# Kernel optimization log

Hardware: AMD Instinct MI355X
Metric: run time of the kernel (lower is better)

Reference implementation:

```python
import jax, jax.numpy as jnp
import numpy as np

N_NODES = 100000
N_EDGES = 1600000
FEATURE = 32
HIDDEN = 64
CLASSES = 10
K = 3  # TAGConv default number of hops


def setup_inputs() -> dict:
    key = jax.random.key(0)
    k1, k2, k3, k4, k5, k6, k7 = jax.random.split(key, 7)
    x = jax.random.normal(k1, (N_NODES, FEATURE), dtype=jnp.float32)
    edge_index = jax.random.randint(k2, (2, N_EDGES), 0, N_NODES, dtype=jnp.int32)
    # TAGConv holds K+1 linear maps (one per hop power) plus a bias.
    s1 = 1.0 / np.sqrt(FEATURE)
    s2 = 1.0 / np.sqrt(HIDDEN)
    W1 = jax.random.uniform(k3, (K + 1, FEATURE, HIDDEN), jnp.float32, -s1, s1)
    b1 = jax.random.uniform(k4, (HIDDEN,), jnp.float32, -s1, s1)
    W2 = jax.random.uniform(k5, (K + 1, HIDDEN, CLASSES), jnp.float32, -s2, s2)
    b2 = jax.random.uniform(k6, (CLASSES,), jnp.float32, -s2, s2)
    return {"x": x, "edge_index": edge_index, "W1": W1, "b1": b1, "W2": W2, "b2": b2}


def _tagconv(x, row, col, norm, W, b):
    # out = sum_k (A_hat^k x) W_k + b, A_hat = D^-1/2 A D^-1/2 (no self loops)
    out = x @ W[0]
    h = x
    for k in range(1, W.shape[0]):
        h = jnp.zeros_like(h).at[col].add(norm[:, None] * h[row])
        out = out + h @ W[k]
    return out + b


def reference(x, edge_index, W1, b1, W2, b2):
    row, col = edge_index[0], edge_index[1]
    n = x.shape[0]
    # gcn_norm with unit edge weights, add_self_loops=False
    deg = jnp.zeros((n,), x.dtype).at[col].add(1.0)
    dinv = jnp.where(deg > 0, jax.lax.rsqrt(jnp.maximum(deg, 1.0)), 0.0)
    norm = dinv[row] * dinv[col]

    h = _tagconv(x, row, col, norm, W1, b1)
    h = jax.nn.relu(h)
    # dropout is identity in eval mode
    h = _tagconv(h, row, col, norm, W2, b2)
    return jax.nn.log_softmax(h, axis=1)
```

## Files before the change

### kernel.cpp

```cpp
#include <hip/hip_runtime.h>

typedef unsigned int uint;
typedef short s8v __attribute__((ext_vector_type(8)));
typedef float f4v __attribute__((ext_vector_type(4)));

#define N_NODES 100000
#define N_EDGES 1600000
#define FEAT 32
#define HID 64
#define NCLS 10

#define BUCKET_SHIFT 8
#define NBUCKET 391
#define NCB 256
#define CHUNK ((N_EDGES + NCB - 1) / NCB)
#define BH_N (NBUCKET * NCB)
#define NB_BH ((BH_N + 255) / 256)
#define CAP 6144
#define LROW 65


__device__ __forceinline__ uint pack_bf16(float lo, float hi) {
    uint a = __float_as_uint(lo);
    uint b = __float_as_uint(hi);
    a = a + 0x7fffu + ((a >> 16) & 1u);
    b = b + 0x7fffu + ((b >> 16) & 1u);
    return (a >> 16) | (b & 0xffff0000u);
}
__device__ __forceinline__ float unp_lo(uint v) { return __uint_as_float(v << 16); }
__device__ __forceinline__ float unp_hi(uint v) { return __uint_as_float(v & 0xffff0000u); }

__device__ __forceinline__ s8v to_s8(uint4 u) {
    union { uint4 u; s8v s; } x;
    x.u = u;
    return x.s;
}


__global__ void bucket_hist(const int* __restrict__ col, int* __restrict__ blockhist) {
    __shared__ int lh[NBUCKET];
    int blk = blockIdx.x;
    for (int i = threadIdx.x; i < NBUCKET; i += 256) lh[i] = 0;
    __syncthreads();
    int e0 = blk * CHUNK;
    int e1 = min(e0 + CHUNK, N_EDGES);
    for (int e = e0 + threadIdx.x; e < e1; e += 256)
        atomicAdd(&lh[col[e] >> BUCKET_SHIFT], 1);
    __syncthreads();
    for (int i = threadIdx.x; i < NBUCKET; i += 256)
        blockhist[i * NCB + blk] = lh[i];
}

__global__ void scanA_kernel(const int* __restrict__ src, int* __restrict__ dst,
                             int* __restrict__ bsum, int n) {
    __shared__ int s[256];
    int gid = blockIdx.x * 256 + threadIdx.x;
    int v = (gid < n) ? src[gid] : 0;
    s[threadIdx.x] = v;
    __syncthreads();
    for (int off = 1; off < 256; off <<= 1) {
        int t = (threadIdx.x >= off) ? s[threadIdx.x - off] : 0;
        __syncthreads();
        s[threadIdx.x] += t;
        __syncthreads();
    }
    if (gid < n) dst[gid] = s[threadIdx.x] - v;
    if (threadIdx.x == 255) bsum[blockIdx.x] = s[255];
}

__global__ void scanB_kernel(int* __restrict__ bsum, int nb) {
    __shared__ int s[512];
    int v = (threadIdx.x < nb) ? bsum[threadIdx.x] : 0;
    s[threadIdx.x] = v;
    __syncthreads();
    for (int off = 1; off < 512; off <<= 1) {
        int t = (threadIdx.x >= off) ? s[threadIdx.x - off] : 0;
        __syncthreads();
        s[threadIdx.x] += t;
        __syncthreads();
    }
    if (threadIdx.x < nb) bsum[threadIdx.x] = s[threadIdx.x] - v;
}

__global__ void scanC_add(int* __restrict__ dst, const int* __restrict__ bsum, int n) {
    int gid = blockIdx.x * 256 + threadIdx.x;
    if (gid < n) dst[gid] += bsum[blockIdx.x];
}

__global__ void bucket_scatter(const int* __restrict__ row, const int* __restrict__ col,
                               const int* __restrict__ base, int* __restrict__ packed) {
    __shared__ int lcnt[NBUCKET];
    __shared__ int lbase[NBUCKET];
    int blk = blockIdx.x;
    for (int i = threadIdx.x; i < NBUCKET; i += 256) {
        lcnt[i] = 0;
        lbase[i] = base[i * NCB + blk];
    }
    __syncthreads();
    int e0 = blk * CHUNK;
    int e1 = min(e0 + CHUNK, N_EDGES);
    for (int e = e0 + threadIdx.x; e < e1; e += 256) {
        int c = col[e];
        int r = row[e];
        int b = c >> BUCKET_SHIFT;
        int pos = lbase[b] + atomicAdd(&lcnt[b], 1);
        packed[pos] = (r << BUCKET_SHIFT) | (c & 255);
    }
}

__global__ void bucket_sort(const int* __restrict__ base, const int* __restrict__ packed,
                            int* __restrict__ rowptr, int* __restrict__ eidx,
                            float* __restrict__ dinv) {
    __shared__ int stage[CAP];
    __shared__ int cnt[256];
    __shared__ int lscan[256];
    int b = blockIdx.x;
    int tid = threadIdx.x;
    int s = base[b * NCB];
    int e = (b == NBUCKET - 1) ? N_EDGES : base[(b + 1) * NCB];
    int m = e - s;
    bool fits = (m <= CAP);
    cnt[tid] = 0;
    __syncthreads();
    for (int i = tid; i < m; i += 256) {
        int p = packed[s + i];
        if (fits) stage[i] = p;
        atomicAdd(&cnt[p & 255], 1);
    }
    __syncthreads();
    int node = (b << BUCKET_SHIFT) + tid;
    int c = cnt[tid];
    if (node < N_NODES) dinv[node] = (c > 0) ? rsqrtf((float)c) : 0.0f;
    lscan[tid] = c;
    __syncthreads();
    for (int off = 1; off < 256; off <<= 1) {
        int t = (tid >= off) ? lscan[tid - off] : 0;
        __syncthreads();
        lscan[tid] += t;
        __syncthreads();
    }
    int excl = lscan[tid] - c;
    if (node < N_NODES) rowptr[node] = s + excl;
    if (b == NBUCKET - 1 && tid == 0) rowptr[N_NODES] = N_EDGES;
    __syncthreads();
    lscan[tid] = excl;
    cnt[tid] = 0;
    __syncthreads();
    for (int i = tid; i < m; i += 256) {
        int p = fits ? stage[i] : packed[s + i];
        int cl = p & 255;
        int pos = lscan[cl] + atomicAdd(&cnt[cl], 1);
        eidx[s + pos] = p >> BUCKET_SHIFT;
    }
}


__global__ void prescale_kernel(const float* __restrict__ x, const float* __restrict__ dinv,
                                uint* __restrict__ t0) {
    int i = blockIdx.x * 256 + threadIdx.x;
    if (i < N_NODES * 16) {
        int node = i >> 4, fp = i & 15;
        float dv = dinv[node];
        t0[i] = pack_bf16(x[node * 32 + 2 * fp] * dv, x[node * 32 + 2 * fp + 1] * dv);
    }
}


template <int WP>
__global__ void gather32_kernel(const int* __restrict__ rowptr, const int* __restrict__ eidx,
                                const float* __restrict__ dinv, const uint* __restrict__ src,
                                uint* __restrict__ pout, uint* __restrict__ preout) {
    int node = (blockIdx.x * blockDim.x + threadIdx.x) >> 6;
    if (node >= N_NODES) return;
    int lane = threadIdx.x & 63;
    int fp = lane & 15;
    int g = lane >> 4;
    int s = rowptr[node], e = rowptr[node + 1];
    float acc0 = 0.0f, acc1 = 0.0f;
    int base = (s & ~3) + g * 4;
    for (int b = base; b < e; b += 16) {
        int4 q = *(const int4*)(eidx + b);
        uint v0 = (b     >= s && b     < e) ? src[q.x * 16 + fp] : 0u;
        uint v1 = (b + 1 >= s && b + 1 < e) ? src[q.y * 16 + fp] : 0u;
        uint v2 = (b + 2 >= s && b + 2 < e) ? src[q.z * 16 + fp] : 0u;
        uint v3 = (b + 3 >= s && b + 3 < e) ? src[q.w * 16 + fp] : 0u;
        acc0 += unp_lo(v0) + unp_lo(v1) + unp_lo(v2) + unp_lo(v3);
        acc1 += unp_hi(v0) + unp_hi(v1) + unp_hi(v2) + unp_hi(v3);
    }
    acc0 += __shfl_xor(acc0, 16);
    acc0 += __shfl_xor(acc0, 32);
    acc1 += __shfl_xor(acc1, 16);
    acc1 += __shfl_xor(acc1, 32);
    if (lane < 16) {
        float dv = dinv[node];
        pout[node * 16 + fp] = pack_bf16(dv * acc0, dv * acc1);
        if (WP) {
            float d2 = dv * dv;
            preout[node * 16 + fp] = pack_bf16(d2 * acc0, d2 * acc1);
        }
    }
}

template <int FINAL>
__global__ void gather16_kernel(const int* __restrict__ rowptr, const int* __restrict__ eidx,
                                const float* __restrict__ dinv, const float* __restrict__ src,
                                const float* __restrict__ add, float* __restrict__ outv) {
    int node = (blockIdx.x * blockDim.x + threadIdx.x) >> 6;
    if (node >= N_NODES) return;
    int lane = threadIdx.x & 63;
    int f = lane & 15;
    int g = lane >> 4;
    int s = rowptr[node], e = rowptr[node + 1];
    float acc = 0.0f;
    int base = (s & ~3) + g * 4;
    for (int b = base; b < e; b += 16) {
        int4 q = *(const int4*)(eidx + b);
        float v0 = (b     >= s && b     < e) ? src[q.x * 16 + f] : 0.0f;
        float v1 = (b + 1 >= s && b + 1 < e) ? src[q.y * 16 + f] : 0.0f;
        float v2 = (b + 2 >= s && b + 2 < e) ? src[q.z * 16 + f] : 0.0f;
        float v3 = (b + 3 >= s && b + 3 < e) ? src[q.w * 16 + f] : 0.0f;
        acc += v0 + v1 + v2 + v3;
    }
    acc += __shfl_xor(acc, 16);
    acc += __shfl_xor(acc, 32);
    float dv = dinv[node];
    float v = add[node * 16 + f] + dv * acc;
    if (!FINAL) {
        if (lane < 16) outv[node * 16 + f] = dv * v;
    } else {
        float l = (f < NCLS) ? v : -1e30f;
        float m = l;
        m = fmaxf(m, __shfl_xor(m, 1));
        m = fmaxf(m, __shfl_xor(m, 2));
        m = fmaxf(m, __shfl_xor(m, 4));
        m = fmaxf(m, __shfl_xor(m, 8));
        float ex = (f < NCLS) ? __expf(l - m) : 0.0f;
        ex += __shfl_xor(ex, 1);
        ex += __shfl_xor(ex, 2);
        ex += __shfl_xor(ex, 4);
        ex += __shfl_xor(ex, 8);
        float ls = logf(ex) + m;
        if (lane < 16 && f < NCLS) outv[node * NCLS + f] = l - ls;
    }
}


__global__ void wfprep_kernel(const float* __restrict__ W1, const float* __restrict__ W2,
                              uint* __restrict__ wf1, uint* __restrict__ wf2) {
    int idx = blockIdx.x * 256 + threadIdx.x;
    if (idx < 4096) {
        int vj = idx & 3, frag = idx >> 2;
        int lane = frag & 63, ks = (frag >> 6) & 3, nt = frag >> 8;
        int g = lane >> 4, c = lane & 15;
        int k0 = ks * 32 + g * 8 + 2 * vj;
        int n = nt * 16 + c;
        wf1[idx] = pack_bf16(W1[k0 * 64 + n], W1[(k0 + 1) * 64 + n]);
    } else if (idx < 6144) {
        int i2 = idx - 4096;
        int vj = i2 & 3, frag = i2 >> 2;
        int lane = frag & 63, ks = (frag >> 6) & 1, nt = frag >> 7;
        int g = lane >> 4, c = lane & 15;
        int k0 = ks * 32 + g * 8 + 2 * vj;
        float v0 = (c < NCLS) ? W2[(nt * HID + k0) * NCLS + c] : 0.0f;
        float v1 = (c < NCLS) ? W2[(nt * HID + k0 + 1) * NCLS + c] : 0.0f;
        wf2[i2] = pack_bf16(v0, v1);
    }
}


__global__ __launch_bounds__(256) void dense_fused(
        const float* __restrict__ x, const uint* __restrict__ p1,
        const uint* __restrict__ p2, const uint* __restrict__ p3,
        const uint* __restrict__ wf1, const uint* __restrict__ wf2,
        const float* __restrict__ b1, const float* __restrict__ b2,
        const float* __restrict__ dinv, float* __restrict__ z, int zstride) {
    __shared__ float hls[4 * 16 * LROW];
    int tid = threadIdx.x;
    int wv = tid >> 6, l = tid & 63, g = l >> 4, c = l & 15;
    float* my = hls + wv * 16 * LROW;
    int row0 = blockIdx.x * 64 + wv * 16;
    int ra = row0 + c;
    int rc = min(ra, N_NODES - 1);

    uint4 au0;
    {
        float4 xa = *(const float4*)(x + rc * 32 + g * 8);
        float4 xb = *(const float4*)(x + rc * 32 + g * 8 + 4);
        au0.x = pack_bf16(xa.x, xa.y);
        au0.y = pack_bf16(xa.z, xa.w);
        au0.z = pack_bf16(xb.x, xb.y);
        au0.w = pack_bf16(xb.z, xb.w);
    }
    uint4 au1 = *(const uint4*)(p1 + rc * 16 + g * 4);
    uint4 au2 = *(const uint4*)(p2 + rc * 16 + g * 4);
    uint4 au3 = *(const uint4*)(p3 + rc * 16 + g * 4);
    s8v a0 = to_s8(au0), a1 = to_s8(au1), a2 = to_s8(au2), a3 = to_s8(au3);

    f4v acc[4];
#pragma unroll
    for (int nt = 0; nt < 4; nt++) {
        f4v ac = {0.f, 0.f, 0.f, 0.f};
        const s8v* wp = (const s8v*)(wf1 + (nt * 4) * 64 * 4 + l * 4);
        ac = __builtin_amdgcn_mfma_f32_16x16x32_bf16(a0, wp[0 * 64], ac, 0, 0, 0);
        ac = __builtin_amdgcn_mfma_f32_16x16x32_bf16(a1, wp[1 * 64], ac, 0, 0, 0);
        ac = __builtin_amdgcn_mfma_f32_16x16x32_bf16(a2, wp[2 * 64], ac, 0, 0, 0);
        ac = __builtin_amdgcn_mfma_f32_16x16x32_bf16(a3, wp[3 * 64], ac, 0, 0, 0);
        acc[nt] = ac;
    }

#pragma unroll
    for (int nt = 0; nt < 4; nt++) {
        float bb = b1[nt * 16 + c];
#pragma unroll
        for (int reg = 0; reg < 4; reg++) {
            my[(4 * g + reg) * LROW + nt * 16 + c] = fmaxf(acc[nt][reg] + bb, 0.0f);
        }
    }
    __syncthreads();

    uint4 b2u[2];
#pragma unroll
    for (int ks = 0; ks < 2; ks++) {
        float4 h0 = *(const float4*)&my[c * LROW + ks * 32 + g * 8];
        float4 h1 = *(const float4*)&my[c * LROW + ks * 32 + g * 8 + 4];
        b2u[ks].x = pack_bf16(h0.x, h0.y);
        b2u[ks].y = pack_bf16(h0.z, h0.w);
        b2u[ks].z = pack_bf16(h1.x, h1.y);
        b2u[ks].w = pack_bf16(h1.z, h1.w);
    }
    s8v h0f = to_s8(b2u[0]), h1f = to_s8(b2u[1]);

    f4v acc2[4];
#pragma unroll
    for (int nt = 0; nt < 4; nt++) {
        f4v ac = {0.f, 0.f, 0.f, 0.f};
        const s8v* wp = (const s8v*)(wf2 + (nt * 2) * 64 * 4 + l * 4);
        ac = __builtin_amdgcn_mfma_f32_16x16x32_bf16(h0f, wp[0 * 64], ac, 0, 0, 0);
        ac = __builtin_amdgcn_mfma_f32_16x16x32_bf16(h1f, wp[1 * 64], ac, 0, 0, 0);
        acc2[nt] = ac;
    }

#pragma unroll
    for (int nt = 0; nt < 4; nt++) {
        float bb = (nt == 0 && c < NCLS) ? b2[c] : 0.0f;
        float* zk = z + (size_t)nt * zstride;
#pragma unroll
        for (int reg = 0; reg < 4; reg++) {
            int rr = row0 + 4 * g + reg;
            if (rr < N_NODES) {
                float v = acc2[nt][reg] + bb;
                if (nt == 3) v *= dinv[rr];
                zk[rr * 16 + c] = v;
            }
        }
    }
}


extern "C" void kernel_launch(void* const* d_in, const int* in_sizes, int n_in,
                              void* d_out, int out_size, void* d_ws, size_t ws_size,
                              hipStream_t stream) {
    const float* x  = (const float*)d_in[0];
    const int*   ei = (const int*)d_in[1];
    const float* W1 = (const float*)d_in[2];
    const float* b1 = (const float*)d_in[3];
    const float* W2 = (const float*)d_in[4];
    const float* b2 = (const float*)d_in[5];
    float* out = (float*)d_out;

    const int* row = ei;
    const int* col = ei + N_EDGES;

    float* w = (float*)d_ws;
    size_t o = 0;
    auto alloc = [&](size_t nel) { float* p = w + o; o += (nel + 63) & ~(size_t)63; return p; };

    int*   rowptr = (int*)alloc(N_NODES + 1);
    int*   bsum   = (int*)alloc(512);
    float* dinv   = alloc(N_NODES);
    uint*  wf1    = (uint*)alloc(4096);
    uint*  wf2    = (uint*)alloc(2048);
    int*   eidx   = (int*)alloc(N_EDGES + 16);
    float* bufA   = alloc((size_t)N_NODES * 32);
    float* bufB   = alloc((size_t)N_NODES * 32);
    float* bufC   = alloc((size_t)N_NODES * 32);
    float* bufD   = alloc((size_t)N_NODES * 32);
    float* h      = alloc((size_t)N_NODES * HID);

    int* blockhist = (int*)bufB;
    int* bhbase    = (int*)bufC;
    int* packed    = (int*)h;

    uint* t0  = (uint*)bufA;
    uint* p1  = (uint*)bufB;
    uint* p1p = (uint*)bufC;
    uint* p2  = (uint*)bufD;
    uint* p2p = (uint*)bufA;
    uint* p3  = (uint*)bufC;
    const int ZS = N_NODES * 16;
    float* z0  = h;
    float* z1  = h + ZS;
    float* z2  = h + 2 * (size_t)ZS;
    float* z3p = h + 3 * (size_t)ZS;
    float* tAp = bufC;
    float* tBp = bufC + ZS;

    const int TB = 256;
    const int gW = (N_NODES * 64) / TB;

    bucket_hist<<<NCB, TB, 0, stream>>>(col, blockhist);
    scanA_kernel<<<NB_BH, TB, 0, stream>>>(blockhist, bhbase, bsum, BH_N);
    scanB_kernel<<<1, 512, 0, stream>>>(bsum, NB_BH);
    scanC_add<<<NB_BH, TB, 0, stream>>>(bhbase, bsum, BH_N);
    bucket_scatter<<<NCB, TB, 0, stream>>>(row, col, bhbase, packed);
    bucket_sort<<<NBUCKET, TB, 0, stream>>>(bhbase, packed, rowptr, eidx, dinv);

    wfprep_kernel<<<24, TB, 0, stream>>>(W1, W2, wf1, wf2);

    prescale_kernel<<<(N_NODES * 16 + TB - 1) / TB, TB, 0, stream>>>(x, dinv, t0);
    gather32_kernel<1><<<gW, TB, 0, stream>>>(rowptr, eidx, dinv, t0,  p1, p1p);
    gather32_kernel<1><<<gW, TB, 0, stream>>>(rowptr, eidx, dinv, p1p, p2, p2p);
    gather32_kernel<0><<<gW, TB, 0, stream>>>(rowptr, eidx, dinv, p2p, p3, nullptr);

    int gF = (N_NODES + 63) / 64;
    dense_fused<<<gF, TB, 0, stream>>>(x, p1, p2, p3, wf1, wf2, b1, b2, dinv, z0, ZS);

    gather16_kernel<0><<<gW, TB, 0, stream>>>(rowptr, eidx, dinv, z3p, z2, tAp);
    gather16_kernel<0><<<gW, TB, 0, stream>>>(rowptr, eidx, dinv, tAp, z1, tBp);
    gather16_kernel<1><<<gW, TB, 0, stream>>>(rowptr, eidx, dinv, tBp, z0, out);
}
```

Before: 346.4 us.

## Store layer-2 propagation buffers in bf16 and pack two nodes per wave

The 16-wide layer-2 intermediates (z0..z3 and the gather ping-pong buffers) are now stored as packed bf16 pairs instead of fp32, halving the bytes moved by the three 16-channel gathers. Each gather wave now processes two nodes with 8 lanes per node, each lane handling two channels, so half as many waves are launched. The dense kernel packs neighbouring-lane outputs with a shuffle before storing. This trades some precision in the output logits for less memory traffic in the random-access gathers.

```diff
diff --git a/kernel.cpp b/kernel.cpp
--- a/kernel.cpp
+++ b/kernel.cpp
@@ -203,44 +203,53 @@
 
 template <int FINAL>
 __global__ void gather16_kernel(const int* __restrict__ rowptr, const int* __restrict__ eidx,
-                                const float* __restrict__ dinv, const float* __restrict__ src,
-                                const float* __restrict__ add, float* __restrict__ outv) {
-    int node = (blockIdx.x * blockDim.x + threadIdx.x) >> 6;
+                                const float* __restrict__ dinv, const uint* __restrict__ src,
+                                const uint* __restrict__ add, void* __restrict__ outv) {
+    int wid = (blockIdx.x * blockDim.x + threadIdx.x) >> 6;
+    int lane = threadIdx.x & 63;
+    int node = wid * 2 + (lane >> 5);
     if (node >= N_NODES) return;
-    int lane = threadIdx.x & 63;
-    int f = lane & 15;
-    int g = lane >> 4;
+    int fp = lane & 7;
+    int g = (lane >> 3) & 3;
     int s = rowptr[node], e = rowptr[node + 1];
-    float acc = 0.0f;
+    float acc0 = 0.0f, acc1 = 0.0f;
     int base = (s & ~3) + g * 4;
     for (int b = base; b < e; b += 16) {
         int4 q = *(const int4*)(eidx + b);
-        float v0 = (b     >= s && b     < e) ? src[q.x * 16 + f] : 0.0f;
-        float v1 = (b + 1 >= s && b + 1 < e) ? src[q.y * 16 + f] : 0.0f;
-        float v2 = (b + 2 >= s && b + 2 < e) ? src[q.z * 16 + f] : 0.0f;
-        float v3 = (b + 3 >= s && b + 3 < e) ? src[q.w * 16 + f] : 0.0f;
-        acc += v0 + v1 + v2 + v3;
-    }
-    acc += __shfl_xor(acc, 16);
-    acc += __shfl_xor(acc, 32);
+        uint v0 = (b     >= s && b     < e) ? src[q.x * 8 + fp] : 0u;
+        uint v1 = (b + 1 >= s && b + 1 < e) ? src[q.y * 8 + fp] : 0u;
+        uint v2 = (b + 2 >= s && b + 2 < e) ? src[q.z * 8 + fp] : 0u;
+        uint v3 = (b + 3 >= s && b + 3 < e) ? src[q.w * 8 + fp] : 0u;
+        acc0 += unp_lo(v0) + unp_lo(v1) + unp_lo(v2) + unp_lo(v3);
+        acc1 += unp_hi(v0) + unp_hi(v1) + unp_hi(v2) + unp_hi(v3);
+    }
+    acc0 += __shfl_xor(acc0, 8);
+    acc0 += __shfl_xor(acc0, 16);
+    acc1 += __shfl_xor(acc1, 8);
+    acc1 += __shfl_xor(acc1, 16);
     float dv = dinv[node];
-    float v = add[node * 16 + f] + dv * acc;
+    uint av = add[node * 8 + fp];
+    float v0 = unp_lo(av) + dv * acc0;
+    float v1 = unp_hi(av) + dv * acc1;
     if (!FINAL) {
-        if (lane < 16) outv[node * 16 + f] = dv * v;
+        if (g == 0) ((uint*)outv)[node * 8 + fp] = pack_bf16(dv * v0, dv * v1);
     } else {
-        float l = (f < NCLS) ? v : -1e30f;
-        float m = l;
+        float l0 = (2 * fp     < NCLS) ? v0 : -1e30f;
+        float l1 = (2 * fp + 1 < NCLS) ? v1 : -1e30f;
+        float m = fmaxf(l0, l1);
         m = fmaxf(m, __shfl_xor(m, 1));
         m = fmaxf(m, __shfl_xor(m, 2));
         m = fmaxf(m, __shfl_xor(m, 4));
-        m = fmaxf(m, __shfl_xor(m, 8));
-        float ex = (f < NCLS) ? __expf(l - m) : 0.0f;
+        float ex = ((2 * fp     < NCLS) ? __expf(l0 - m) : 0.0f)
+                 + ((2 * fp + 1 < NCLS) ? __expf(l1 - m) : 0.0f);
         ex += __shfl_xor(ex, 1);
         ex += __shfl_xor(ex, 2);
         ex += __shfl_xor(ex, 4);
-        ex += __shfl_xor(ex, 8);
         float ls = logf(ex) + m;
-        if (lane < 16 && f < NCLS) outv[node * NCLS + f] = l - ls;
+        if (g == 0 && fp < 5) {
+            float2 o = {l0 - ls, l1 - ls};
+            *(float2*)((float*)outv + (size_t)node * 10 + 2 * fp) = o;
+        }
     }
 }
 
@@ -273,7 +282,7 @@
         const uint* __restrict__ p2, const uint* __restrict__ p3,
         const uint* __restrict__ wf1, const uint* __restrict__ wf2,
         const float* __restrict__ b1, const float* __restrict__ b2,
-        const float* __restrict__ dinv, float* __restrict__ z, int zstride) {
+        const float* __restrict__ dinv, uint* __restrict__ z, int zstride) {
     __shared__ float hls[4 * 16 * LROW];
     int tid = threadIdx.x;
     int wv = tid >> 6, l = tid & 63, g = l >> 4, c = l & 15;
@@ -343,14 +352,15 @@
 #pragma unroll
     for (int nt = 0; nt < 4; nt++) {
         float bb = (nt == 0 && c < NCLS) ? b2[c] : 0.0f;
-        float* zk = z + (size_t)nt * zstride;
+        uint* zk = z + (size_t)nt * zstride;
 #pragma unroll
         for (int reg = 0; reg < 4; reg++) {
             int rr = row0 + 4 * g + reg;
-            if (rr < N_NODES) {
-                float v = acc2[nt][reg] + bb;
-                if (nt == 3) v *= dinv[rr];
-                zk[rr * 16 + c] = v;
+            float v = acc2[nt][reg] + bb;
+            if (nt == 3) v *= dinv[min(rr, N_NODES - 1)];
+            float vn = __shfl_xor(v, 1);
+            if (rr < N_NODES && (c & 1) == 0) {
+                zk[rr * 8 + (c >> 1)] = pack_bf16(v, vn);
             }
         }
     }
@@ -397,16 +407,17 @@
     uint* p2  = (uint*)bufD;
     uint* p2p = (uint*)bufA;
     uint* p3  = (uint*)bufC;
-    const int ZS = N_NODES * 16;
-    float* z0  = h;
-    float* z1  = h + ZS;
-    float* z2  = h + 2 * (size_t)ZS;
-    float* z3p = h + 3 * (size_t)ZS;
-    float* tAp = bufC;
-    float* tBp = bufC + ZS;
+    const int ZS = N_NODES * 8;
+    uint* z0  = (uint*)h;
+    uint* z1  = (uint*)h + ZS;
+    uint* z2  = (uint*)h + 2 * (size_t)ZS;
+    uint* z3p = (uint*)h + 3 * (size_t)ZS;
+    uint* tAp = (uint*)bufC;
+    uint* tBp = (uint*)bufC + ZS;
 
     const int TB = 256;
     const int gW = (N_NODES * 64) / TB;
+    const int gW2 = ((N_NODES + 1) / 2 * 64 + TB - 1) / TB;
 
     bucket_hist<<<NCB, TB, 0, stream>>>(col, blockhist);
     scanA_kernel<<<NB_BH, TB, 0, stream>>>(blockhist, bhbase, bsum, BH_N);
@@ -425,7 +436,7 @@
     int gF = (N_NODES + 63) / 64;
     dense_fused<<<gF, TB, 0, stream>>>(x, p1, p2, p3, wf1, wf2, b1, b2, dinv, z0, ZS);
 
-    gather16_kernel<0><<<gW, TB, 0, stream>>>(rowptr, eidx, dinv, z3p, z2, tAp);
-    gather16_kernel<0><<<gW, TB, 0, stream>>>(rowptr, eidx, dinv, tAp, z1, tBp);
-    gather16_kernel<1><<<gW, TB, 0, stream>>>(rowptr, eidx, dinv, tBp, z0, out);
-}
+    gather16_kernel<0><<<gW2, TB, 0, stream>>>(rowptr, eidx, dinv, z3p, z2, tAp);
+    gather16_kernel<0><<<gW2, TB, 0, stream>>>(rowptr, eidx, dinv, tAp, z1, tBp);
+    gather16_kernel<1><<<gW2, TB, 0, stream>>>(rowptr, eidx, dinv, tBp, z0, out);
+}
```

Result: faster. 285.1 us, median of 2 (-17.7%).
